# Kernel tuning notes

Hardware: AMD Instinct MI355X
Metric: run time of the kernel (lower is better)

Reference implementation:

```python
import jax, jax.numpy as jnp
import numpy as np

BOS_ID = 0
EOS_ID = 1


def setup_inputs() -> dict:
    key = jax.random.key(0)
    ks = jax.random.split(key, 16)
    B, L, F = 64, 200, 512
    H, E, A = 512, 512, 512
    V, T = 50257, 21
    D = E + F  # rnn input_dim
    s = lambda n: 1.0 / np.sqrt(n)
    ref = jax.random.randint(ks[0], (B, T), 2, V, dtype=jnp.int32)
    ref = ref.at[:, 0].set(BOS_ID).at[:, -1].set(EOS_ID)
    return {
        "encoder_output": jax.random.normal(ks[1], (B, L, F), jnp.float32),
        "decoder_init_hidden": jax.random.normal(ks[2], (1, B, H), jnp.float32),
        "encoding_mask": jnp.ones((B, L, 1), jnp.float32),
        "temp_seg": jax.random.uniform(ks[3], (B, 2), jnp.float32),
        "embed_table": jax.random.normal(ks[4], (V, E), jnp.float32) * 0.02,
        "W_ih": jax.random.normal(ks[5], (3 * H, D), jnp.float32) * s(D),
        "W_hh": jax.random.normal(ks[6], (3 * H, H), jnp.float32) * s(H),
        "b_ih": jnp.zeros((3 * H,), jnp.float32),
        "b_hh": jnp.zeros((3 * H,), jnp.float32),
        "Wa_enc": jax.random.normal(ks[7], (F, A), jnp.float32) * s(F),
        "Wa_h": jax.random.normal(ks[8], (H, A), jnp.float32) * s(H),
        "v_att": jax.random.normal(ks[9], (A,), jnp.float32) * s(A),
        "W_out": jax.random.normal(ks[10], (V, H), jnp.float32) * s(H),
        "b_out": jnp.zeros((V,), jnp.float32),
        "ref_caption": ref,
    }


def reference(encoder_output, decoder_init_hidden, encoding_mask, temp_seg,
              embed_table, W_ih, W_hh, b_ih, b_hh,
              Wa_enc, Wa_h, v_att, W_out, b_out, ref_caption):
    # Teacher-forced training forward of RNNSeqDecoder (GRU, 1 layer).
    B, T = ref_caption.shape
    V = embed_table.shape[0]
    enc_proj = jnp.einsum('blf,fa->bla', encoder_output, Wa_enc)  # precompute attn enc term
    mask = encoding_mask[..., 0]  # (B,L)
    h0 = decoder_init_hidden[0]   # (B,H)

    def step(h, word):
        emb = embed_table[word]                                        # (B,E)
        # additive attention over encoder states (masked)
        score = jnp.einsum('bla,a->bl', jnp.tanh(enc_proj + (h @ Wa_h)[:, None, :]), v_att)
        score = jnp.where(mask > 0, score, -1e9)
        attn = jax.nn.softmax(score, axis=1)
        ctx = jnp.einsum('bl,blf->bf', attn, encoder_output)           # (B,F)
        x = jnp.concatenate([emb, ctx], axis=1)                        # (B,E+F)
        # PyTorch GRU cell
        gi = x @ W_ih.T + b_ih
        gh = h @ W_hh.T + b_hh
        i_r, i_z, i_n = jnp.split(gi, 3, axis=1)
        h_r, h_z, h_n = jnp.split(gh, 3, axis=1)
        r = jax.nn.sigmoid(i_r + h_r)
        z = jax.nn.sigmoid(i_z + h_z)
        n = jnp.tanh(i_n + r * h_n)
        h_new = (1.0 - z) * n + z * h
        logp = jax.nn.log_softmax(h_new @ W_out.T + b_out, axis=1)     # (B,V)
        return h_new, logp

    _, logps = jax.lax.scan(step, h0, ref_caption[:, :-1].T)           # (T-1,B,V)
    first = jnp.zeros((B, 1, V), logps.dtype)  # BOS_ID == 0, matches torch.zeros(...) + BOS_ID
    caption_prob = jnp.concatenate([first, jnp.swapaxes(logps, 0, 1)], axis=1)  # (B,T,V)
    return caption_prob
```

## Files before the change

### kernel.cpp

```cpp
#include <hip/hip_runtime.h>
#include <stdint.h>
#include <stddef.h>

#define B_ 64
#define L_ 200
#define F_ 512
#define H_ 512
#define A_ 512
#define E_ 512
#define V_ 50257
#define PADV 50304
#define T_ 21
#define D_ 1024
#define NBLK32 1572
#define BH (B_ * H_)
#define BD (B_ * D_)
#define NROW 1280

typedef __attribute__((ext_vector_type(8))) short short8;
typedef __attribute__((ext_vector_type(4))) float f32x4;

__device__ __forceinline__ unsigned short f2b(float f) {
  unsigned int u = __builtin_bit_cast(unsigned int, f);
  u += 0x7FFFu + ((u >> 16) & 1u);
  return (unsigned short)(u >> 16);
}
__device__ __forceinline__ float b2f(unsigned short s) {
  unsigned int u = ((unsigned int)s) << 16;
  return __builtin_bit_cast(float, u);
}
__device__ __forceinline__ f32x4 mfma16(short8 a, short8 b, f32x4 c) {
  return __builtin_amdgcn_mfma_f32_16x16x32_bf16(a, b, c, 0, 0, 0);
}
__device__ __forceinline__ int hsoff(int b, int j) {
  return (((b >> 4) * 16 + (j >> 5)) * 64 + (((j >> 3) & 3) * 16 + (b & 15))) * 8 + (j & 7);
}
__device__ __forceinline__ int xoff(int b, int k) {
  return (((b >> 4) * 32 + (k >> 5)) * 64 + (((k >> 3) & 3) * 16 + (b & 15))) * 8 + (k & 7);
}


__device__ void cvt_dev(const float* __restrict__ src, unsigned short* __restrict__ dst,
                        int n4, int vbid, int nblk) {
  int i = vbid * 256 + threadIdx.x;
  int stride = nblk * 256;
  const float4* s4 = (const float4*)src;
  ushort4* d4 = (ushort4*)dst;
  for (; i < n4; i += stride) {
    float4 v = s4[i];
    ushort4 o;
    o.x = f2b(v.x); o.y = f2b(v.y); o.z = f2b(v.z); o.w = f2b(v.w);
    d4[i] = o;
  }
}

__device__ void wfrag_dev(const float* __restrict__ src, unsigned short* __restrict__ dst,
                          int K, int rt) {
  int r15 = threadIdx.x & 15;
  int row = rt * 16 + r15;
  int nch = K >> 3;
  int kpw = K >> 5;
  for (int kc = threadIdx.x >> 4; kc < nch; kc += 16) {
    const float4* s = (const float4*)(src + (size_t)row * K + kc * 8);
    float4 x = s[0], y = s[1];
    short8 o;
    o[0] = f2b(x.x); o[1] = f2b(x.y); o[2] = f2b(x.z); o[3] = f2b(x.w);
    o[4] = f2b(y.x); o[5] = f2b(y.y); o[6] = f2b(y.z); o[7] = f2b(y.w);
    *(short8*)(dst + ((size_t)(rt * kpw + (kc >> 2)) * 64 + ((kc & 3) * 16 + r15)) * 8) = o;
  }
}

__global__ __launch_bounds__(256) void k_setupA(const float* __restrict__ Wout, unsigned short* __restrict__ Wb,
                                                const float* __restrict__ enc, unsigned short* __restrict__ encb,
                                                const float* __restrict__ Wih, unsigned short* __restrict__ Wfih,
                                                const float* __restrict__ Whh, unsigned short* __restrict__ Wfhh,
                                                const float* __restrict__ Waenc, unsigned short* __restrict__ WaTb,
                                                const float* __restrict__ Wah, float* __restrict__ WahT32,
                                                const float* __restrict__ dih, unsigned short* __restrict__ hsAll,
                                                const int* __restrict__ ref, const float* __restrict__ et,
                                                unsigned short* __restrict__ xAll) {
  __shared__ float tile[64][65];
  int bid = blockIdx.x;
  int tid = threadIdx.x;
  if (bid < 4096) {
    cvt_dev(Wout, Wb, V_ * H_ / 4, bid, 4096);
  } else if (bid < 6144) {
    cvt_dev(enc, encb, B_ * L_ * F_ / 4, bid - 4096, 2048);
  } else if (bid < 6240) {
    wfrag_dev(Wih, Wfih, 1024, bid - 6144);
  } else if (bid < 6336) {
    wfrag_dev(Whh, Wfhh, 512, bid - 6240);
  } else if (bid < 6400) {
    int q = bid - 6336;
    int cb = (q & 7) * 64, rb = (q >> 3) * 64;
    int tx = tid & 63, ty = tid >> 6;
#pragma unroll
    for (int i = 0; i < 16; ++i) {
      int r = ty * 16 + i;
      tile[r][tx] = Waenc[(size_t)(rb + r) * 512 + cb + tx];
    }
    __syncthreads();
#pragma unroll
    for (int i = 0; i < 16; ++i) {
      int c = ty * 16 + i;
      WaTb[(size_t)(cb + c) * 512 + rb + tx] = f2b(tile[tx][c]);
    }
  } else if (bid < 6464) {
    int q = bid - 6400;
    int cb = (q & 7) * 64, rb = (q >> 3) * 64;
    int tx = tid & 63, ty = tid >> 6;
#pragma unroll
    for (int i = 0; i < 16; ++i) {
      int r = ty * 16 + i;
      tile[r][tx] = Wah[(size_t)(rb + r) * 512 + cb + tx];
    }
    __syncthreads();
#pragma unroll
    for (int i = 0; i < 16; ++i) {
      int c = ty * 16 + i;
      WahT32[(size_t)(cb + c) * 512 + rb + tx] = tile[tx][c];
    }
  } else if (bid < 6528) {
    int b = bid - 6464;
    for (int j = tid; j < H_; j += 256)
      hsAll[hsoff(b, j)] = f2b(dih[(size_t)b * H_ + j]);
  } else {
    int q = bid - 6528;
    int b = q & 63, tp = q >> 6;
    if (tid < 64) {
      int word = ref[b * T_ + tp];
      const float* er = et + (size_t)word * E_;
      unsigned short* dst = xAll + (size_t)tp * BD;
      int c = tid;
      const float4* s = (const float4*)(er + c * 8);
      float4 x = s[0], y = s[1];
      short8 o;
      o[0] = f2b(x.x); o[1] = f2b(x.y); o[2] = f2b(x.z); o[3] = f2b(x.w);
      o[4] = f2b(y.x); o[5] = f2b(y.y); o[6] = f2b(y.z); o[7] = f2b(y.w);
      *(short8*)(dst + xoff(b, c * 8)) = o;
    }
  }
}

__global__ __launch_bounds__(256) void k_setupB(const float* __restrict__ WahT32,
                                                unsigned short* __restrict__ Wahf,
                                                const unsigned short* __restrict__ encb,
                                                const unsigned short* __restrict__ WaTb,
                                                unsigned short* __restrict__ epb) {
  __shared__ unsigned short al[32768];
  int bid = blockIdx.x;
  int tid = threadIdx.x;
  if (bid < 32) {
    wfrag_dev(WahT32, Wahf, 512, bid);
    return;
  }
  size_t rowbase = (size_t)(bid - 32) * 64;
  for (int idx = tid; idx < 4096; idx += 256) {
    int row = idx >> 6, seg = idx & 63;
    unsigned char* dp = (unsigned char*)al + row * 1024 + ((seg * 16) ^ ((row & 7) << 4));
    *(short8*)dp = *(const short8*)(encb + (rowbase + row) * F_ + seg * 8);
  }
  __syncthreads();
  int w = tid >> 6, lane = tid & 63, ln15 = lane & 15, g = lane >> 4;
  int sw = (ln15 & 7) << 4;
  const unsigned char* alb = (const unsigned char*)al;
  int mrow = w * 16 + ln15;
  for (int nt = 0; nt < 32; ++nt) {
    f32x4 acc = {0.f, 0.f, 0.f, 0.f};
    const unsigned short* brow = WaTb + (size_t)(nt * 16 + ln15) * F_ + 8 * g;
#pragma unroll 4
    for (int kk = 0; kk < 16; ++kk) {
      short8 bf = *(const short8*)(brow + kk * 32);
      short8 af = *(const short8*)(alb + mrow * 1024 + ((kk * 64 + 16 * g) ^ sw));
      acc = mfma16(af, bf, acc);
    }
#pragma unroll
    for (int r = 0; r < 4; ++r) {
      size_t m = rowbase + w * 16 + 4 * g + r;
      epb[m * A_ + nt * 16 + ln15] = f2b(acc[r]);
    }
  }
}


__global__ __launch_bounds__(256) void k_hwgh(const unsigned short* __restrict__ Wahf,
                                              const unsigned short* __restrict__ Wfhh,
                                              const unsigned short* __restrict__ hs,
                                              float* __restrict__ hw,
                                              float* __restrict__ ghG) {
  int blk = blockIdx.x;
  int w = threadIdx.x >> 6, lane = threadIdx.x & 63;
  int ln15 = lane & 15, g = lane >> 4;
  if (blk < 32) {
    f32x4 acc = {0.f, 0.f, 0.f, 0.f};
#pragma unroll 4
    for (int kk = 0; kk < 16; ++kk) {
      short8 av = *(const short8*)(Wahf + (((size_t)blk * 16 + kk) * 64 + lane) * 8);
      short8 hv = *(const short8*)(hs + (((size_t)w * 16 + kk) * 64 + lane) * 8);
      acc = mfma16(av, hv, acc);
    }
#pragma unroll
    for (int r = 0; r < 4; ++r) {
      int a = blk * 16 + 4 * g + r;
      int b = w * 16 + ln15;
      hw[(size_t)b * 512 + a] = acc[r];
    }
  } else {
    int jt = blk - 32;
    f32x4 acc = {0.f, 0.f, 0.f, 0.f};
#pragma unroll
    for (int kk = 0; kk < 16; ++kk) {
      short8 wv = *(const short8*)(Wfhh + (((size_t)jt * 16 + kk) * 64 + lane) * 8);
      short8 hv = *(const short8*)(hs + (((size_t)w * 16 + kk) * 64 + lane) * 8);
      acc = mfma16(wv, hv, acc);
    }
#pragma unroll
    for (int r = 0; r < 4; ++r) {
      int j = jt * 16 + 4 * g + r;
      int b = w * 16 + ln15;
      ghG[(size_t)j * B_ + b] = acc[r];
    }
  }
}


__global__ __launch_bounds__(1024) void k_attB(const float* __restrict__ mask,
                                               const float* __restrict__ vatt,
                                               const unsigned short* __restrict__ encb,
                                               const unsigned short* __restrict__ epb,
                                               const float* __restrict__ hw,
                                               unsigned short* __restrict__ xplane) {
  __shared__ float sm[208];
  __shared__ float ctxp[16][F_];
  __shared__ float ctxF[F_];
  int b = blockIdx.x;
  int tid = threadIdx.x;
  int w = tid >> 6, lane = tid & 63;
  float hwv[8], vv[8];
  {
    const float4* hp = (const float4*)(hw + (size_t)b * 512 + lane * 8);
    const float4* vp = (const float4*)(vatt + lane * 8);
    float4 h0 = hp[0], h1 = hp[1], v0 = vp[0], v1 = vp[1];
    hwv[0] = h0.x; hwv[1] = h0.y; hwv[2] = h0.z; hwv[3] = h0.w;
    hwv[4] = h1.x; hwv[5] = h1.y; hwv[6] = h1.z; hwv[7] = h1.w;
    vv[0] = v0.x; vv[1] = v0.y; vv[2] = v0.z; vv[3] = v0.w;
    vv[4] = v1.x; vv[5] = v1.y; vv[6] = v1.z; vv[7] = v1.w;
  }
  for (int l = w; l < L_; l += 16) {
    short8 ev = *(const short8*)(epb + ((size_t)(b * L_ + l)) * 512 + lane * 8);
    float p = 0.f;
#pragma unroll
    for (int j = 0; j < 8; ++j) {
      float x = b2f((unsigned short)ev[j]) + hwv[j];
      float e2 = __expf(x + x);
      p = fmaf(1.f - 2.f / (e2 + 1.f), vv[j], p);
    }
    for (int o = 1; o < 64; o <<= 1) p += __shfl_xor(p, o);
    if (lane == 0) {
      float mk = mask[b * L_ + l];
      sm[l] = (mk > 0.f) ? p : -1e9f;
    }
  }
  __syncthreads();
  if (tid < 64) {
    float m = -1e30f;
    for (int l = tid; l < L_; l += 64) m = fmaxf(m, sm[l]);
    for (int o = 1; o < 64; o <<= 1) m = fmaxf(m, __shfl_xor(m, o));
    float s = 0.f;
    for (int l = tid; l < L_; l += 64) s += __expf(sm[l] - m);
    for (int o = 1; o < 64; o <<= 1) s += __shfl_xor(s, o);
    float inv = 1.f / s;
    for (int l = tid; l < L_; l += 64) sm[l] = __expf(sm[l] - m) * inv;
  }
  __syncthreads();
  float c[8] = {0.f, 0.f, 0.f, 0.f, 0.f, 0.f, 0.f, 0.f};
  for (int l = w; l < L_; l += 16) {
    float wgt = sm[l];
    short8 ev = *(const short8*)(encb + ((size_t)(b * L_ + l)) * 512 + lane * 8);
#pragma unroll
    for (int j = 0; j < 8; ++j) c[j] = fmaf(wgt, b2f((unsigned short)ev[j]), c[j]);
  }
#pragma unroll
  for (int j = 0; j < 8; ++j) ctxp[w][lane * 8 + j] = c[j];
  __syncthreads();
  if (tid < 512) {
    float s = 0.f;
#pragma unroll
    for (int q = 0; q < 16; ++q) s += ctxp[q][tid];
    ctxF[tid] = s;
  }
  __syncthreads();
  if (tid < 64) {
    short8 o;
#pragma unroll
    for (int j = 0; j < 8; ++j) o[j] = f2b(ctxF[tid * 8 + j]);
    *(short8*)(xplane + xoff(b, E_ + tid * 8)) = o;
  }
}


__global__ __launch_bounds__(256) void k_stepB(const unsigned short* __restrict__ Wfih,
                                               const float* __restrict__ bih,
                                               const float* __restrict__ bhh,
                                               const unsigned short* __restrict__ xplane,
                                               const float* __restrict__ ghG,
                                               const float* __restrict__ hBold,
                                               unsigned short* __restrict__ hsnew,
                                               float* __restrict__ hBnew) {
  int bx = blockIdx.x;
  int w = threadIdx.x >> 6, lane = threadIdx.x & 63;
  int ln15 = lane & 15, g = lane >> 4;
  f32x4 z4 = {0.f, 0.f, 0.f, 0.f};
  f32x4 aIr = z4, aIz = z4, aIn = z4;
#pragma unroll 2
  for (int kk = 0; kk < 32; ++kk) {
    short8 xv = *(const short8*)(xplane + (((size_t)w * 32 + kk) * 64 + lane) * 8);
    aIr = mfma16(*(const short8*)(Wfih + (((size_t)(0 * 32 + bx) * 32 + kk) * 64 + lane) * 8), xv, aIr);
    aIz = mfma16(*(const short8*)(Wfih + (((size_t)(32 + bx) * 32 + kk) * 64 + lane) * 8), xv, aIz);
    aIn = mfma16(*(const short8*)(Wfih + (((size_t)(64 + bx) * 32 + kk) * 64 + lane) * 8), xv, aIn);
  }
  int jb = bx * 16;
#pragma unroll
  for (int r = 0; r < 4; ++r) {
    int j = jb + 4 * g + r;
    int b = w * 16 + ln15;
    float ir = aIr[r] + bih[j];
    float iz = aIz[r] + bih[512 + j];
    float in_ = aIn[r] + bih[1024 + j];
    float hrv = ghG[(size_t)j * B_ + b] + bhh[j];
    float hzv = ghG[(size_t)(512 + j) * B_ + b] + bhh[512 + j];
    float hnv = ghG[(size_t)(1024 + j) * B_ + b] + bhh[1024 + j];
    float rg = 1.f / (1.f + __expf(-(ir + hrv)));
    float zg = 1.f / (1.f + __expf(-(iz + hzv)));
    float e2 = __expf(2.f * (in_ + rg * hnv));
    float ng = 1.f - 2.f / (e2 + 1.f);
    float ho = hBold[(size_t)b * H_ + j];
    float hv = (1.f - zg) * ng + zg * ho;
    hBnew[(size_t)b * H_ + j] = hv;
    hsnew[hsoff(b, j)] = f2b(hv);
  }
}


__global__ __launch_bounds__(256) void k_blog(const unsigned short* __restrict__ Wb,
                                              const float* __restrict__ bout,
                                              const unsigned short* __restrict__ hsAll,
                                              float* __restrict__ out,
                                              unsigned short* __restrict__ lws, int mode) {
  __shared__ unsigned short tile[2][64][40];
  int tid = threadIdx.x;
  int w = tid >> 6, lane = tid & 63, ln15 = lane & 15, g = lane >> 4;
  int ch = w & 1, mh = w >> 1;
  int vcol = blockIdx.x * 32 + ch * 16 + ln15;
  bool vok = vcol < V_;
  int vr = vok ? vcol : (V_ - 1);
  const unsigned short* brow = Wb + (size_t)vr * H_ + 8 * g;
  short8 wb[16];
#pragma unroll
  for (int kk = 0; kk < 16; ++kk) wb[kk] = *(const short8*)(brow + kk * 32);
  float bo = bout[vr];
  int row = tid >> 2, seg = tid & 3;

  for (int t = 0; t < T_ - 1; ++t) {
    const unsigned short* hp = hsAll + (size_t)(t + 1) * BH;
    int buf = t & 1;
    __builtin_amdgcn_s_setprio(1);
    f32x4 z4 = {0.f, 0.f, 0.f, 0.f};
    f32x4 acc0 = z4, acc1 = z4;
#pragma unroll
    for (int kk = 0; kk < 16; ++kk) {
      short8 a0 = *(const short8*)(hp + (((mh * 2 + 0) * 16 + kk) * 64 + lane) * 8);
      short8 a1 = *(const short8*)(hp + (((mh * 2 + 1) * 16 + kk) * 64 + lane) * 8);
      acc0 = mfma16(a0, wb[kk], acc0);
      acc1 = mfma16(a1, wb[kk], acc1);
    }
    __builtin_amdgcn_s_setprio(0);
#pragma unroll
    for (int r = 0; r < 4; ++r) {
      int bi0 = (mh * 2 + 0) * 16 + 4 * g + r;
      int bi1 = (mh * 2 + 1) * 16 + 4 * g + r;
      int col = ch * 16 + ln15;
      tile[buf][bi0][col] = vok ? f2b(acc0[r] + bo) : f2b(-1e30f);
      tile[buf][bi1][col] = vok ? f2b(acc1[r] + bo) : f2b(-1e30f);
    }
    __syncthreads();
    int cb = blockIdx.x * 32 + seg * 8;
    if (mode == 1) {
      short8 sv = *(const short8*)&tile[buf][row][seg * 8];
      *(short8*)(lws + ((size_t)t * 64 + row) * PADV + cb) = sv;
    } else {
      short8 sv = *(const short8*)&tile[buf][row][seg * 8];
      float* orow = out + ((size_t)row * T_ + (t + 1)) * V_ + cb;
      if (cb + 8 <= V_) {
#pragma unroll
        for (int i = 0; i < 8; ++i) orow[i] = b2f((unsigned short)sv[i]);
      } else {
        for (int i = 0; i < 8; ++i)
          if (cb + i < V_) orow[i] = b2f((unsigned short)sv[i]);
      }
    }
  }
}


__global__ __launch_bounds__(512) void k_lsefin(const unsigned short* __restrict__ lws,
                                                float* __restrict__ out) {
  __shared__ unsigned short srow[PADV];
  __shared__ float lm[512], ls[512];
  __shared__ float lvs;
  int bid = blockIdx.x;
  int tid = threadIdx.x;
  if (bid >= NROW) {
    int b = bid - NROW;
    float* o = out + (size_t)b * T_ * V_;
    float4 z = make_float4(0.f, 0.f, 0.f, 0.f);
    for (int i = tid; i < 12564; i += 512) *(float4*)(o + i * 4) = z;
    if (tid == 0) o[50256] = 0.f;
    return;
  }
  int rho = bid;
  int tp = rho >> 6, b = rho & 63;
  const unsigned short* src = lws + (size_t)(tp * 64 + b) * PADV;
  float* o = out + ((size_t)b * T_ + (tp + 1)) * V_;
  float m = -1e30f, s = 0.f;
  for (int i = tid; i < PADV / 8; i += 512) {
    short8 sv = *(const short8*)(src + i * 8);
    *(short8*)(srow + i * 8) = sv;
    float x0 = b2f((unsigned short)sv[0]), x1 = b2f((unsigned short)sv[1]);
    float x2 = b2f((unsigned short)sv[2]), x3 = b2f((unsigned short)sv[3]);
    float x4 = b2f((unsigned short)sv[4]), x5 = b2f((unsigned short)sv[5]);
    float x6 = b2f((unsigned short)sv[6]), x7 = b2f((unsigned short)sv[7]);
    float cm = fmaxf(fmaxf(fmaxf(x0, x1), fmaxf(x2, x3)), fmaxf(fmaxf(x4, x5), fmaxf(x6, x7)));
    float cs = __expf(x0 - cm) + __expf(x1 - cm) + __expf(x2 - cm) + __expf(x3 - cm) +
               __expf(x4 - cm) + __expf(x5 - cm) + __expf(x6 - cm) + __expf(x7 - cm);
    float nm = fmaxf(m, cm);
    s = s * __expf(m - nm) + cs * __expf(cm - nm);
    m = nm;
  }
  lm[tid] = m; ls[tid] = s;
  __syncthreads();
  for (int o2 = 256; o2 > 0; o2 >>= 1) {
    if (tid < o2) {
      float m2 = lm[tid + o2], s2 = ls[tid + o2];
      float nm = fmaxf(lm[tid], m2);
      ls[tid] = ls[tid] * __expf(lm[tid] - nm) + s2 * __expf(m2 - nm);
      lm[tid] = nm;
    }
    __syncthreads();
  }
  if (tid == 0) lvs = lm[0] + logf(ls[0]);
  __syncthreads();
  float Lv = lvs;
  for (int i = tid; i < 6282; i += 512) {
    short8 sv = *(const short8*)(srow + i * 8);
    float4 v0, v1;
    v0.x = b2f((unsigned short)sv[0]) - Lv; v0.y = b2f((unsigned short)sv[1]) - Lv;
    v0.z = b2f((unsigned short)sv[2]) - Lv; v0.w = b2f((unsigned short)sv[3]) - Lv;
    v1.x = b2f((unsigned short)sv[4]) - Lv; v1.y = b2f((unsigned short)sv[5]) - Lv;
    v1.z = b2f((unsigned short)sv[6]) - Lv; v1.w = b2f((unsigned short)sv[7]) - Lv;
    *(float4*)(o + i * 8) = v0;
    *(float4*)(o + i * 8 + 4) = v1;
  }
  if (tid == 0) o[50256] = b2f(srow[50256]) - Lv;
}

__global__ __launch_bounds__(256) void k_lsefin0(float* __restrict__ out) {
  __shared__ float lm[256], ls[256];
  __shared__ float lvs;
  int bid = blockIdx.x;
  int tid = threadIdx.x;
  if (bid >= NROW) {
    int b = bid - NROW;
    float* o = out + (size_t)b * T_ * V_;
    for (int v = tid; v < V_; v += 256) o[v] = 0.f;
    return;
  }
  int rho = bid;
  int tp = rho >> 6, b = rho & 63;
  float* o = out + ((size_t)b * T_ + (tp + 1)) * V_;
  float m = -1e30f, s = 0.f;
  for (int v = tid; v < V_; v += 256) {
    float x = o[v];
    float nm = fmaxf(m, x);
    s = s * __expf(m - nm) + __expf(x - nm);
    m = nm;
  }
  lm[tid] = m; ls[tid] = s;
  __syncthreads();
  for (int o2 = 128; o2 > 0; o2 >>= 1) {
    if (tid < o2) {
      float m2 = lm[tid + o2], s2 = ls[tid + o2];
      float nm = fmaxf(lm[tid], m2);
      ls[tid] = ls[tid] * __expf(lm[tid] - nm) + s2 * __expf(m2 - nm);
      lm[tid] = nm;
    }
    __syncthreads();
  }
  if (tid == 0) lvs = lm[0] + logf(ls[0]);
  __syncthreads();
  float Lv = lvs;
  for (int v = tid; v < V_; v += 256) o[v] -= Lv;
}


extern "C" void kernel_launch(void* const* d_in, const int* in_sizes, int n_in,
                              void* d_out, int out_size, void* d_ws, size_t ws_size,
                              hipStream_t stream) {
  const float* enc   = (const float*)d_in[0];
  const float* dih   = (const float*)d_in[1];
  const float* mask  = (const float*)d_in[2];
  const float* et    = (const float*)d_in[4];
  const float* Wih   = (const float*)d_in[5];
  const float* Whh   = (const float*)d_in[6];
  const float* bih   = (const float*)d_in[7];
  const float* bhh   = (const float*)d_in[8];
  const float* Waenc = (const float*)d_in[9];
  const float* Wah   = (const float*)d_in[10];
  const float* vatt  = (const float*)d_in[11];
  const float* Wout  = (const float*)d_in[12];
  const float* bout  = (const float*)d_in[13];
  const int*   ref   = (const int*)d_in[14];
  float* out = (float*)d_out;

  char* w = (char*)d_ws;
  size_t o = 0;
  unsigned short* Wb    = (unsigned short*)(w + o); o += (size_t)V_ * H_ * 2;
  unsigned short* Wfih  = (unsigned short*)(w + o); o += (size_t)1536 * 1024 * 2;
  unsigned short* Wfhh  = (unsigned short*)(w + o); o += (size_t)1536 * 512 * 2;
  unsigned short* WaTb  = (unsigned short*)(w + o); o += (size_t)512 * 512 * 2;
  unsigned short* Wahf  = (unsigned short*)(w + o); o += (size_t)512 * 512 * 2;
  float* WahT32 = (float*)(w + o); o += (size_t)512 * 512 * 4;
  unsigned short* encb  = (unsigned short*)(w + o); o += (size_t)B_ * L_ * F_ * 2;
  unsigned short* epb   = (unsigned short*)(w + o); o += (size_t)B_ * L_ * A_ * 2;
  unsigned short* xAll  = (unsigned short*)(w + o); o += (size_t)20 * BD * 2;
  unsigned short* hsAll = (unsigned short*)(w + o); o += (size_t)T_ * BH * 2;
  float* hBAll = (float*)(w + o); o += (size_t)T_ * BH * 4;
  float* ghG   = (float*)(w + o); o += (size_t)1536 * B_ * 4;
  float* hw    = (float*)(w + o); o += (size_t)B_ * A_ * 4 + 256;
  unsigned short* lws = (unsigned short*)(w + o);
  size_t need = o + (size_t)NROW * PADV * 2;
  int mode = (ws_size >= need) ? 1 : 0;

  k_setupA<<<7808, 256, 0, stream>>>(Wout, Wb, enc, encb, Wih, Wfih, Whh, Wfhh,
                                     Waenc, WaTb, Wah, WahT32, dih, hsAll, ref, et, xAll);
  k_setupB<<<232, 256, 0, stream>>>(WahT32, Wahf, encb, WaTb, epb);

  for (int t = 0; t < T_ - 1; ++t) {
    const float* hB_t = (t == 0) ? dih : (hBAll + (size_t)t * BH);
    float* hB_n = hBAll + (size_t)(t + 1) * BH;
    const unsigned short* hs_t = hsAll + (size_t)t * BH;
    unsigned short* hs_n = hsAll + (size_t)(t + 1) * BH;
    unsigned short* xp = xAll + (size_t)t * BD;
    k_hwgh<<<128, 256, 0, stream>>>(Wahf, Wfhh, hs_t, hw, ghG);
    k_attB<<<64, 1024, 0, stream>>>(mask, vatt, encb, epb, hw, xp);
    k_stepB<<<32, 256, 0, stream>>>(Wfih, bih, bhh, xp, ghG, hB_t, hs_n, hB_n);
  }
  k_blog<<<NBLK32, 256, 0, stream>>>(Wb, bout, hsAll, out, lws, mode);
  if (mode == 1) k_lsefin<<<NROW + 64, 512, 0, stream>>>(lws, out);
  else k_lsefin0<<<NROW + 64, 256, 0, stream>>>(out);
}
```

Baseline: 1.304 ms.

## Fuse recurrent decoder steps into one persistent cooperative kernel with grid barriers

```diff
diff --git a/kernel.cpp b/kernel.cpp
--- a/kernel.cpp
+++ b/kernel.cpp
@@ -16,6 +16,7 @@
 #define BH (B_ * H_)
 #define BD (B_ * D_)
 #define NROW 1280
+#define NBP 128
 
 typedef __attribute__((ext_vector_type(8))) short short8;
 typedef __attribute__((ext_vector_type(4))) float f32x4;
@@ -37,6 +38,25 @@
 }
 __device__ __forceinline__ int xoff(int b, int k) {
   return (((b >> 4) * 32 + (k >> 5)) * 64 + (((k >> 3) & 3) * 16 + (b & 15))) * 8 + (k & 7);
+}
+
+__device__ __forceinline__ float aldf(const float* p) {
+  return __hip_atomic_load(p, __ATOMIC_RELAXED, __HIP_MEMORY_SCOPE_AGENT);
+}
+__device__ __forceinline__ void astf(float* p, float v) {
+  __hip_atomic_store(p, v, __ATOMIC_RELAXED, __HIP_MEMORY_SCOPE_AGENT);
+}
+__device__ __forceinline__ unsigned long long aldu(const void* p) {
+  return __hip_atomic_load((const unsigned long long*)p, __ATOMIC_RELAXED, __HIP_MEMORY_SCOPE_AGENT);
+}
+__device__ __forceinline__ void astu(void* p, unsigned long long v) {
+  __hip_atomic_store((unsigned long long*)p, v, __ATOMIC_RELAXED, __HIP_MEMORY_SCOPE_AGENT);
+}
+__device__ __forceinline__ short8 ald16(const unsigned short* p) {
+  union { unsigned long long u[2]; short8 s; } t;
+  t.u[0] = aldu(p);
+  t.u[1] = aldu(p + 4);
+  return t.s;
 }
 
 
@@ -146,10 +166,12 @@
                                                 unsigned short* __restrict__ Wahf,
                                                 const unsigned short* __restrict__ encb,
                                                 const unsigned short* __restrict__ WaTb,
-                                                unsigned short* __restrict__ epb) {
+                                                unsigned short* __restrict__ epb,
+                                                unsigned int* __restrict__ cnt) {
   __shared__ unsigned short al[32768];
   int bid = blockIdx.x;
   int tid = threadIdx.x;
+  if (bid == 0 && tid == 0) *cnt = 0;
   if (bid < 32) {
     wfrag_dev(WahT32, Wahf, 512, bid);
     return;
@@ -179,6 +201,176 @@
       size_t m = rowbase + w * 16 + 4 * g + r;
       epb[m * A_ + nt * 16 + ln15] = f2b(acc[r]);
     }
+  }
+}
+
+
+struct RecPP {
+  const float* mask; const float* vatt;
+  const unsigned short* encb; const unsigned short* epb;
+  const unsigned short* Wahf; const unsigned short* Wfhh; const unsigned short* Wfih;
+  const float* bih; const float* bhh;
+  const float* dih;
+  unsigned short* hsAll; float* hBAll; unsigned short* xAll;
+  float* hw; float* ghG;
+  unsigned int* cnt;
+};
+
+__device__ __forceinline__ void gbar(unsigned int* cnt, unsigned int target) {
+  __syncthreads();
+  if (threadIdx.x == 0) {
+    __hip_atomic_fetch_add(cnt, 1u, __ATOMIC_RELAXED, __HIP_MEMORY_SCOPE_AGENT);
+    while (__hip_atomic_load(cnt, __ATOMIC_RELAXED, __HIP_MEMORY_SCOPE_AGENT) < target)
+      __builtin_amdgcn_s_sleep(8);
+  }
+  __syncthreads();
+}
+
+__global__ __launch_bounds__(512) void k_rec2(RecPP P) {
+  __shared__ float sm[208];
+  __shared__ float ctxp[8][F_];
+  __shared__ float ctxF[F_];
+  int blk = blockIdx.x;
+  int tid = threadIdx.x;
+  unsigned int tgt = 0;
+
+  for (int t = 0; t < T_ - 1; ++t) {
+    const unsigned short* hs_t = P.hsAll + (size_t)t * BH;
+    unsigned short* xp = P.xAll + (size_t)t * BD;
+    if (tid < 256) {
+      int w = tid >> 6, lane = tid & 63, ln15 = lane & 15, g = lane >> 4;
+      if (blk < 32) {
+        f32x4 acc = {0.f, 0.f, 0.f, 0.f};
+#pragma unroll 4
+        for (int kk = 0; kk < 16; ++kk) {
+          short8 av = *(const short8*)(P.Wahf + (((size_t)blk * 16 + kk) * 64 + lane) * 8);
+          short8 hv = ald16(hs_t + (((size_t)w * 16 + kk) * 64 + lane) * 8);
+          acc = mfma16(av, hv, acc);
+        }
+#pragma unroll
+        for (int r = 0; r < 4; ++r)
+          astf(P.hw + (size_t)(w * 16 + ln15) * 512 + blk * 16 + 4 * g + r, acc[r]);
+      } else {
+        int jt = blk - 32;
+        f32x4 acc = {0.f, 0.f, 0.f, 0.f};
+#pragma unroll 4
+        for (int kk = 0; kk < 16; ++kk) {
+          short8 wv = *(const short8*)(P.Wfhh + (((size_t)jt * 16 + kk) * 64 + lane) * 8);
+          short8 hv = ald16(hs_t + (((size_t)w * 16 + kk) * 64 + lane) * 8);
+          acc = mfma16(wv, hv, acc);
+        }
+#pragma unroll
+        for (int r = 0; r < 4; ++r)
+          astf(P.ghG + (size_t)(jt * 16 + 4 * g + r) * B_ + w * 16 + ln15, acc[r]);
+      }
+    }
+    tgt += NBP; gbar(P.cnt, tgt);
+
+    if (blk < 64) {
+      int b = blk;
+      int w = tid >> 6, lane = tid & 63;
+      float hwv[8], vv[8];
+#pragma unroll
+      for (int j = 0; j < 8; ++j) {
+        hwv[j] = aldf(P.hw + (size_t)b * 512 + lane * 8 + j);
+        vv[j] = P.vatt[lane * 8 + j];
+      }
+      for (int l = w; l < L_; l += 8) {
+        short8 ev = *(const short8*)(P.epb + ((size_t)(b * L_ + l)) * 512 + lane * 8);
+        float p = 0.f;
+#pragma unroll
+        for (int j = 0; j < 8; ++j) {
+          float x = b2f((unsigned short)ev[j]) + hwv[j];
+          float e2 = __expf(x + x);
+          p = fmaf(1.f - 2.f / (e2 + 1.f), vv[j], p);
+        }
+        for (int o = 1; o < 64; o <<= 1) p += __shfl_xor(p, o);
+        if (lane == 0) {
+          float mk = P.mask[b * L_ + l];
+          sm[l] = (mk > 0.f) ? p : -1e9f;
+        }
+      }
+      __syncthreads();
+      if (tid < 64) {
+        float m = -1e30f;
+        for (int l = tid; l < L_; l += 64) m = fmaxf(m, sm[l]);
+        for (int o = 1; o < 64; o <<= 1) m = fmaxf(m, __shfl_xor(m, o));
+        float s = 0.f;
+        for (int l = tid; l < L_; l += 64) s += __expf(sm[l] - m);
+        for (int o = 1; o < 64; o <<= 1) s += __shfl_xor(s, o);
+        float inv = 1.f / s;
+        for (int l = tid; l < L_; l += 64) sm[l] = __expf(sm[l] - m) * inv;
+      }
+      __syncthreads();
+      float c[8] = {0.f, 0.f, 0.f, 0.f, 0.f, 0.f, 0.f, 0.f};
+      for (int l = w; l < L_; l += 8) {
+        float wgt = sm[l];
+        short8 ev = *(const short8*)(P.encb + ((size_t)(b * L_ + l)) * 512 + lane * 8);
+#pragma unroll
+        for (int j = 0; j < 8; ++j) c[j] = fmaf(wgt, b2f((unsigned short)ev[j]), c[j]);
+      }
+#pragma unroll
+      for (int j = 0; j < 8; ++j) ctxp[w][lane * 8 + j] = c[j];
+      __syncthreads();
+      if (tid < 512) {
+        float s = 0.f;
+#pragma unroll
+        for (int q = 0; q < 8; ++q) s += ctxp[q][tid];
+        ctxF[tid] = s;
+      }
+      __syncthreads();
+      if (tid < 64) {
+        unsigned long long lo = 0, hi = 0;
+#pragma unroll
+        for (int j = 0; j < 4; ++j) lo |= (unsigned long long)f2b(ctxF[tid * 8 + j]) << (16 * j);
+#pragma unroll
+        for (int j = 0; j < 4; ++j) hi |= (unsigned long long)f2b(ctxF[tid * 8 + 4 + j]) << (16 * j);
+        unsigned short* dst = xp + xoff(b, E_ + tid * 8);
+        astu(dst, lo);
+        astu(dst + 4, hi);
+      }
+    }
+    tgt += NBP; gbar(P.cnt, tgt);
+
+    if (blk < 32 && tid < 256) {
+      int bx = blk;
+      int w = tid >> 6, lane = tid & 63, ln15 = lane & 15, g = lane >> 4;
+      const float* hBold = (t == 0) ? P.dih : (P.hBAll + (size_t)t * BH);
+      float* hBnew = P.hBAll + (size_t)(t + 1) * BH;
+      unsigned short* hsnew = P.hsAll + (size_t)(t + 1) * BH;
+      f32x4 z4 = {0.f, 0.f, 0.f, 0.f};
+      f32x4 aIr = z4, aIz = z4, aIn = z4;
+#pragma unroll 2
+      for (int kk = 0; kk < 32; ++kk) {
+        short8 xv = ald16(xp + (((size_t)w * 32 + kk) * 64 + lane) * 8);
+        aIr = mfma16(*(const short8*)(P.Wfih + (((size_t)(0 * 32 + bx) * 32 + kk) * 64 + lane) * 8), xv, aIr);
+        aIz = mfma16(*(const short8*)(P.Wfih + (((size_t)(32 + bx) * 32 + kk) * 64 + lane) * 8), xv, aIz);
+        aIn = mfma16(*(const short8*)(P.Wfih + (((size_t)(64 + bx) * 32 + kk) * 64 + lane) * 8), xv, aIn);
+      }
+      int jb = bx * 16;
+      int b = w * 16 + ln15;
+      unsigned long long pk = 0;
+#pragma unroll
+      for (int r = 0; r < 4; ++r) {
+        int j = jb + 4 * g + r;
+        float ir = aIr[r] + P.bih[j];
+        float iz = aIz[r] + P.bih[512 + j];
+        float in_ = aIn[r] + P.bih[1024 + j];
+        float hrv = aldf(P.ghG + (size_t)j * B_ + b) + P.bhh[j];
+        float hzv = aldf(P.ghG + (size_t)(512 + j) * B_ + b) + P.bhh[512 + j];
+        float hnv = aldf(P.ghG + (size_t)(1024 + j) * B_ + b) + P.bhh[1024 + j];
+        float rg = 1.f / (1.f + __expf(-(ir + hrv)));
+        float zg = 1.f / (1.f + __expf(-(iz + hzv)));
+        float e2 = __expf(2.f * (in_ + rg * hnv));
+        float ng = 1.f - 2.f / (e2 + 1.f);
+        float ho = aldf(hBold + (size_t)b * H_ + j);
+        float hv = (1.f - zg) * ng + zg * ho;
+        astf(hBnew + (size_t)b * H_ + j, hv);
+        pk |= (unsigned long long)f2b(hv) << (16 * r);
+      }
+      astu(hsnew + hsoff(b, jb + 4 * g), pk);
+    }
+    tgt += NBP; gbar(P.cnt, tgt);
   }
 }
 
@@ -200,11 +392,8 @@
       acc = mfma16(av, hv, acc);
     }
 #pragma unroll
-    for (int r = 0; r < 4; ++r) {
-      int a = blk * 16 + 4 * g + r;
-      int b = w * 16 + ln15;
-      hw[(size_t)b * 512 + a] = acc[r];
-    }
+    for (int r = 0; r < 4; ++r)
+      hw[(size_t)(w * 16 + ln15) * 512 + blk * 16 + 4 * g + r] = acc[r];
   } else {
     int jt = blk - 32;
     f32x4 acc = {0.f, 0.f, 0.f, 0.f};
@@ -215,14 +404,10 @@
       acc = mfma16(wv, hv, acc);
     }
 #pragma unroll
-    for (int r = 0; r < 4; ++r) {
-      int j = jt * 16 + 4 * g + r;
-      int b = w * 16 + ln15;
-      ghG[(size_t)j * B_ + b] = acc[r];
-    }
-  }
-}
-
+    for (int r = 0; r < 4; ++r)
+      ghG[(size_t)(jt * 16 + 4 * g + r) * B_ + w * 16 + ln15] = acc[r];
+  }
+}
 
 __global__ __launch_bounds__(1024) void k_attB(const float* __restrict__ mask,
                                                const float* __restrict__ vatt,
@@ -298,7 +483,6 @@
   }
 }
 
-
 __global__ __launch_bounds__(256) void k_stepB(const unsigned short* __restrict__ Wfih,
                                                const float* __restrict__ bih,
                                                const float* __restrict__ bhh,
@@ -536,24 +720,39 @@
   unsigned short* hsAll = (unsigned short*)(w + o); o += (size_t)T_ * BH * 2;
   float* hBAll = (float*)(w + o); o += (size_t)T_ * BH * 4;
   float* ghG   = (float*)(w + o); o += (size_t)1536 * B_ * 4;
-  float* hw    = (float*)(w + o); o += (size_t)B_ * A_ * 4 + 256;
+  float* hw    = (float*)(w + o); o += (size_t)B_ * A_ * 4;
+  unsigned int* cnt = (unsigned int*)(w + o); o += 256;
   unsigned short* lws = (unsigned short*)(w + o);
   size_t need = o + (size_t)NROW * PADV * 2;
   int mode = (ws_size >= need) ? 1 : 0;
 
   k_setupA<<<7808, 256, 0, stream>>>(Wout, Wb, enc, encb, Wih, Wfih, Whh, Wfhh,
                                      Waenc, WaTb, Wah, WahT32, dih, hsAll, ref, et, xAll);
-  k_setupB<<<232, 256, 0, stream>>>(WahT32, Wahf, encb, WaTb, epb);
-
-  for (int t = 0; t < T_ - 1; ++t) {
-    const float* hB_t = (t == 0) ? dih : (hBAll + (size_t)t * BH);
-    float* hB_n = hBAll + (size_t)(t + 1) * BH;
-    const unsigned short* hs_t = hsAll + (size_t)t * BH;
-    unsigned short* hs_n = hsAll + (size_t)(t + 1) * BH;
-    unsigned short* xp = xAll + (size_t)t * BD;
-    k_hwgh<<<128, 256, 0, stream>>>(Wahf, Wfhh, hs_t, hw, ghG);
-    k_attB<<<64, 1024, 0, stream>>>(mask, vatt, encb, epb, hw, xp);
-    k_stepB<<<32, 256, 0, stream>>>(Wfih, bih, bhh, xp, ghG, hB_t, hs_n, hB_n);
+  k_setupB<<<232, 256, 0, stream>>>(WahT32, Wahf, encb, WaTb, epb, cnt);
+
+  RecPP rp;
+  rp.mask = mask; rp.vatt = vatt;
+  rp.encb = encb; rp.epb = epb;
+  rp.Wahf = Wahf; rp.Wfhh = Wfhh; rp.Wfih = Wfih;
+  rp.bih = bih; rp.bhh = bhh;
+  rp.dih = dih;
+  rp.hsAll = hsAll; rp.hBAll = hBAll; rp.xAll = xAll;
+  rp.hw = hw; rp.ghG = ghG;
+  rp.cnt = cnt;
+  void* args[] = {&rp};
+  hipError_t err = hipLaunchCooperativeKernel((const void*)k_rec2, dim3(NBP), dim3(512),
+                                              args, 0, stream);
+  if (err != hipSuccess) {
+    for (int t = 0; t < T_ - 1; ++t) {
+      const float* hB_t = (t == 0) ? dih : (hBAll + (size_t)t * BH);
+      float* hB_n = hBAll + (size_t)(t + 1) * BH;
+      const unsigned short* hs_t = hsAll + (size_t)t * BH;
+      unsigned short* hs_n = hsAll + (size_t)(t + 1) * BH;
+      unsigned short* xp = xAll + (size_t)t * BD;
+      k_hwgh<<<128, 256, 0, stream>>>(Wahf, Wfhh, hs_t, hw, ghG);
+      k_attB<<<64, 1024, 0, stream>>>(mask, vatt, encb, epb, hw, xp);
+      k_stepB<<<32, 256, 0, stream>>>(Wfih, bih, bhh, xp, ghG, hB_t, hs_n, hB_n);
+    }
   }
   k_blog<<<NBLK32, 256, 0, stream>>>(Wb, bout, hsAll, out, lws, mode);
   if (mode == 1) k_lsefin<<<NROW + 64, 512, 0, stream>>>(lws, out);
```

Measured after the change: 1.715 ms. 1.32x slower.
